# Kernel tuning notes

Hardware: AMD Instinct MI355X
Metric: run time of the kernel (lower is better)

## Reference

```python
import jax, jax.numpy as jnp
import numpy as np

R = 4  # box-filter radius (init kwarg 'radious')


def _diff(c, r, axis):
    # c: cumulative sum along `axis`; returns box-sum along that axis.
    n = c.shape[axis]
    sl = lambda a, b: jax.lax.slice_in_dim(c, a, b, axis=axis)
    left = sl(r, 2 * r + 1)
    middle = sl(2 * r + 1, n) - sl(0, n - 2 * r - 1)
    right = sl(n - 1, n) - sl(n - 2 * r - 1, n - r - 1)
    return jnp.concatenate([left, middle, right], axis=axis)


def _box_filter(x, r):
    # cumsum along H (axis 2) -> windowed diff along H,
    # then cumsum along W (axis 3) -> windowed diff along W.
    return _diff(jnp.cumsum(_diff(jnp.cumsum(x, axis=2), r, axis=2), axis=3), r, axis=3)


def setup_inputs() -> dict:
    key = jax.random.key(0)
    x = jax.random.uniform(key, (8, 3, 1024, 1024), dtype=jnp.float32)
    return {"x": x}


def reference(x) -> jnp.ndarray:
    return _box_filter(x, R)
```

## Files before the change

kernel.cpp:

```cpp
#include <hip/hip_runtime.h>


constexpr int H = 1024, W = 1024;
constexpr int RAD = 4;
constexpr int CHUNK = 16;
constexpr int NCHUNK = H / CHUNK;
constexpr int NIMG = 24;
constexpr int NROWS = CHUNK + 2 * RAD + 1;
constexpr int TPB = 256;

__global__ __launch_bounds__(TPB) void box9_kernel(const float* __restrict__ x,
                                                   float* __restrict__ out) {
    __shared__ float4 Vs[2][TPB + 2];

    const int t     = threadIdx.x;
    const int bid   = blockIdx.x;
    const int chunk = bid & (NCHUNK - 1);
    const int img   = bid >> 6;

    const float* xp = x   + (size_t)img * (H * W) + 4 * t;
    float*       op = out + (size_t)img * (H * W) + 4 * t;
    const int h0 = chunk * CHUNK;

    if (t == 0) {
        Vs[0][0] = make_float4(0.f, 0.f, 0.f, 0.f);
        Vs[1][0] = make_float4(0.f, 0.f, 0.f, 0.f);
    }
    if (t == TPB - 1) {
        Vs[0][TPB + 1] = make_float4(0.f, 0.f, 0.f, 0.f);
        Vs[1][TPB + 1] = make_float4(0.f, 0.f, 0.f, 0.f);
    }

    float4 r[NROWS];
#pragma unroll
    for (int j = 0; j < NROWS; ++j) {
        const int row = h0 - RAD + j;
        r[j] = ((unsigned)row < (unsigned)H)
             ? *reinterpret_cast<const float4*>(xp + (size_t)row * W)
             : make_float4(0.f, 0.f, 0.f, 0.f);
    }

    float4 V = make_float4(0.f, 0.f, 0.f, 0.f);
#pragma unroll
    for (int j = 0; j < 9; ++j) {
        V.x += r[j].x; V.y += r[j].y; V.z += r[j].z; V.w += r[j].w;
    }

#pragma unroll
    for (int j = 0; j < CHUNK; ++j) {
        const int buf = j & 1;
        Vs[buf][t + 1] = V;
        __syncthreads();
        const float4 VL = Vs[buf][t];
        const float4 VR = Vs[buf][t + 2];

        const float T   = V.x + V.y + V.z + V.w;
        const float ls3 = VL.w;
        const float ls2 = ls3 + VL.z;
        const float ls1 = ls2 + VL.y;
        const float lT  = ls1 + VL.x;
        const float rp0 = VR.x;
        const float rp1 = rp0 + VR.y;
        const float rp2 = rp1 + VR.z;
        const float rT  = rp2 + VR.w;

        float4 o;
        o.x = lT  + T + rp0;
        o.y = ls1 + T + rp1;
        o.z = ls2 + T + rp2;
        o.w = ls3 + T + rT;
        *reinterpret_cast<float4*>(op + (size_t)(h0 + j) * W) = o;

        V.x += r[j + 9].x - r[j].x;
        V.y += r[j + 9].y - r[j].y;
        V.z += r[j + 9].z - r[j].z;
        V.w += r[j + 9].w - r[j].w;
    }
}

extern "C" void kernel_launch(void* const* d_in, const int* in_sizes, int n_in,
                              void* d_out, int out_size, void* d_ws, size_t ws_size,
                              hipStream_t stream) {
    const float* x   = (const float*)d_in[0];
    float*       out = (float*)d_out;
    const int n_blocks = NIMG * NCHUNK;
    box9_kernel<<<dim3(n_blocks), dim3(TPB), 0, stream>>>(x, out);
}
```

Baseline: 42.37 us.

## Replace per-row shared-memory halo exchange with wave shuffles and single barrier

Each thread now computes all 16 vertical window sums up front and keeps them in registers. Neighbor sums come from cross-lane shuffles inside each 64-lane wave, and only wave-boundary lanes exchange through small shared arrays. This cuts the 16 per-row __syncthreads barriers to one. The cost is higher register pressure from the 16 extra float4 values, which may lower occupancy, plus 8 shuffles per row.

```diff
diff --git a/kernel.cpp b/kernel.cpp
--- a/kernel.cpp
+++ b/kernel.cpp
@@ -11,25 +11,22 @@
 
 __global__ __launch_bounds__(TPB) void box9_kernel(const float* __restrict__ x,
                                                    float* __restrict__ out) {
-    __shared__ float4 Vs[2][TPB + 2];
+    __shared__ float4 L63s[5][CHUNK];
+    __shared__ float4 L0s[5][CHUNK];
 
-    const int t     = threadIdx.x;
-    const int bid   = blockIdx.x;
+    const int t    = threadIdx.x;
+    const int lane = t & 63;
+    const int wv   = t >> 6;
+    const int bid  = blockIdx.x;
     const int chunk = bid & (NCHUNK - 1);
     const int img   = bid >> 6;
+
+    if (t < CHUNK)               L63s[0][t] = make_float4(0.f, 0.f, 0.f, 0.f);
+    else if (t < 2 * CHUNK)      L0s[4][t - CHUNK] = make_float4(0.f, 0.f, 0.f, 0.f);
 
     const float* xp = x   + (size_t)img * (H * W) + 4 * t;
     float*       op = out + (size_t)img * (H * W) + 4 * t;
     const int h0 = chunk * CHUNK;
-
-    if (t == 0) {
-        Vs[0][0] = make_float4(0.f, 0.f, 0.f, 0.f);
-        Vs[1][0] = make_float4(0.f, 0.f, 0.f, 0.f);
-    }
-    if (t == TPB - 1) {
-        Vs[0][TPB + 1] = make_float4(0.f, 0.f, 0.f, 0.f);
-        Vs[1][TPB + 1] = make_float4(0.f, 0.f, 0.f, 0.f);
-    }
 
     float4 r[NROWS];
 #pragma unroll
@@ -46,15 +43,36 @@
         V.x += r[j].x; V.y += r[j].y; V.z += r[j].z; V.w += r[j].w;
     }
 
+    float4 V16[CHUNK];
 #pragma unroll
     for (int j = 0; j < CHUNK; ++j) {
-        const int buf = j & 1;
-        Vs[buf][t + 1] = V;
-        __syncthreads();
-        const float4 VL = Vs[buf][t];
-        const float4 VR = Vs[buf][t + 2];
+        V16[j] = V;
+        if (lane == 0)  L0s[wv][j]      = V;
+        if (lane == 63) L63s[wv + 1][j] = V;
+        V.x += r[j + 9].x - r[j].x;
+        V.y += r[j + 9].y - r[j].y;
+        V.z += r[j + 9].z - r[j].z;
+        V.w += r[j + 9].w - r[j].w;
+    }
 
-        const float T   = V.x + V.y + V.z + V.w;
+    __syncthreads();
+
+#pragma unroll
+    for (int j = 0; j < CHUNK; ++j) {
+        const float4 Vj = V16[j];
+        float4 VL, VR;
+        VL.x = __shfl(Vj.x, lane - 1);
+        VL.y = __shfl(Vj.y, lane - 1);
+        VL.z = __shfl(Vj.z, lane - 1);
+        VL.w = __shfl(Vj.w, lane - 1);
+        VR.x = __shfl(Vj.x, lane + 1);
+        VR.y = __shfl(Vj.y, lane + 1);
+        VR.z = __shfl(Vj.z, lane + 1);
+        VR.w = __shfl(Vj.w, lane + 1);
+        if (lane == 0)  VL = L63s[wv][j];
+        if (lane == 63) VR = L0s[wv + 1][j];
+
+        const float T   = Vj.x + Vj.y + Vj.z + Vj.w;
         const float ls3 = VL.w;
         const float ls2 = ls3 + VL.z;
         const float ls1 = ls2 + VL.y;
@@ -70,11 +88,6 @@
         o.z = ls2 + T + rp2;
         o.w = ls3 + T + rT;
         *reinterpret_cast<float4*>(op + (size_t)(h0 + j) * W) = o;
-
-        V.x += r[j + 9].x - r[j].x;
-        V.y += r[j + 9].y - r[j].y;
-        V.z += r[j + 9].z - r[j].z;
-        V.w += r[j + 9].w - r[j].w;
     }
 }
 
```

Result: slower. 44.19 us (+4.3%).

## Replace LDS exchange and block barriers with wave shuffles and halo loads

Applied to the files above, without the earlier changes.

Each wavefront now handles an independent 256-column strip, and neighbour column sums are exchanged with __shfl instead of shared memory plus __syncthreads. Edge lanes load an extra halo float4 column and keep a second running sum so strip boundaries stay correct. This removes a block-wide barrier per output row, at the cost of redundant halo loads and extra registers for the r2 array.

```diff
diff --git a/kernel.cpp b/kernel.cpp
--- a/kernel.cpp
+++ b/kernel.cpp
@@ -5,54 +5,66 @@
 constexpr int RAD = 4;
 constexpr int CHUNK = 16;
 constexpr int NCHUNK = H / CHUNK;
+constexpr int NSTRIP = 4;
 constexpr int NIMG = 24;
 constexpr int NROWS = CHUNK + 2 * RAD + 1;
-constexpr int TPB = 256;
+constexpr int HW = H * W;
 
-__global__ __launch_bounds__(TPB) void box9_kernel(const float* __restrict__ x,
+__global__ __launch_bounds__(256) void box9_kernel(const float* __restrict__ x,
                                                    float* __restrict__ out) {
-    __shared__ float4 Vs[2][TPB + 2];
+    const int lane = threadIdx.x & 63;
+    const int wid  = blockIdx.x * 4 + (threadIdx.x >> 6);
 
-    const int t     = threadIdx.x;
-    const int bid   = blockIdx.x;
-    const int chunk = bid & (NCHUNK - 1);
-    const int img   = bid >> 6;
+    const int chunk = wid & (NCHUNK - 1);
+    const int rest  = wid >> 6;
+    const int strip = rest & (NSTRIP - 1);
+    const int img   = rest >> 2;
 
-    const float* xp = x   + (size_t)img * (H * W) + 4 * t;
-    float*       op = out + (size_t)img * (H * W) + 4 * t;
+    const int cs = strip * 256 + 4 * lane;
+    const float* xp = x   + (size_t)img * HW + cs;
+    float*       op = out + (size_t)img * HW + cs;
+
+    const bool isL  = (lane == 0);
+    const bool isR  = (lane == 63);
+    const bool has2 = (isL && strip > 0) || (isR && strip < NSTRIP - 1);
+    const int  cs2  = isL ? (cs - 4) : (cs + 4);
+    const float* xp2 = x + (size_t)img * HW + (has2 ? cs2 : cs);
+
     const int h0 = chunk * CHUNK;
 
-    if (t == 0) {
-        Vs[0][0] = make_float4(0.f, 0.f, 0.f, 0.f);
-        Vs[1][0] = make_float4(0.f, 0.f, 0.f, 0.f);
-    }
-    if (t == TPB - 1) {
-        Vs[0][TPB + 1] = make_float4(0.f, 0.f, 0.f, 0.f);
-        Vs[1][TPB + 1] = make_float4(0.f, 0.f, 0.f, 0.f);
+    float4 r[NROWS], r2[NROWS];
+#pragma unroll
+    for (int j = 0; j < NROWS; ++j) {
+        const int  row = h0 - RAD + j;
+        const bool rok = (unsigned)row < (unsigned)H;
+        r[j] = rok ? *reinterpret_cast<const float4*>(xp + (size_t)row * W)
+                   : make_float4(0.f, 0.f, 0.f, 0.f);
+        r2[j] = (rok && has2)
+              ? *reinterpret_cast<const float4*>(xp2 + (size_t)row * W)
+              : make_float4(0.f, 0.f, 0.f, 0.f);
     }
 
-    float4 r[NROWS];
-#pragma unroll
-    for (int j = 0; j < NROWS; ++j) {
-        const int row = h0 - RAD + j;
-        r[j] = ((unsigned)row < (unsigned)H)
-             ? *reinterpret_cast<const float4*>(xp + (size_t)row * W)
-             : make_float4(0.f, 0.f, 0.f, 0.f);
-    }
-
-    float4 V = make_float4(0.f, 0.f, 0.f, 0.f);
+    float4 V  = make_float4(0.f, 0.f, 0.f, 0.f);
+    float4 V2 = make_float4(0.f, 0.f, 0.f, 0.f);
 #pragma unroll
     for (int j = 0; j < 9; ++j) {
-        V.x += r[j].x; V.y += r[j].y; V.z += r[j].z; V.w += r[j].w;
+        V.x  += r[j].x;  V.y  += r[j].y;  V.z  += r[j].z;  V.w  += r[j].w;
+        V2.x += r2[j].x; V2.y += r2[j].y; V2.z += r2[j].z; V2.w += r2[j].w;
     }
 
 #pragma unroll
     for (int j = 0; j < CHUNK; ++j) {
-        const int buf = j & 1;
-        Vs[buf][t + 1] = V;
-        __syncthreads();
-        const float4 VL = Vs[buf][t];
-        const float4 VR = Vs[buf][t + 2];
+        float4 VL, VR;
+        VL.x = __shfl(V.x, lane - 1);
+        VL.y = __shfl(V.y, lane - 1);
+        VL.z = __shfl(V.z, lane - 1);
+        VL.w = __shfl(V.w, lane - 1);
+        VR.x = __shfl(V.x, lane + 1);
+        VR.y = __shfl(V.y, lane + 1);
+        VR.z = __shfl(V.z, lane + 1);
+        VR.w = __shfl(V.w, lane + 1);
+        if (isL) VL = V2;
+        if (isR) VR = V2;
 
         const float T   = V.x + V.y + V.z + V.w;
         const float ls3 = VL.w;
@@ -71,10 +83,14 @@
         o.w = ls3 + T + rT;
         *reinterpret_cast<float4*>(op + (size_t)(h0 + j) * W) = o;
 
-        V.x += r[j + 9].x - r[j].x;
-        V.y += r[j + 9].y - r[j].y;
-        V.z += r[j + 9].z - r[j].z;
-        V.w += r[j + 9].w - r[j].w;
+        V.x  += r[j + 9].x  - r[j].x;
+        V.y  += r[j + 9].y  - r[j].y;
+        V.z  += r[j + 9].z  - r[j].z;
+        V.w  += r[j + 9].w  - r[j].w;
+        V2.x += r2[j + 9].x - r2[j].x;
+        V2.y += r2[j + 9].y - r2[j].y;
+        V2.z += r2[j + 9].z - r2[j].z;
+        V2.w += r2[j + 9].w - r2[j].w;
     }
 }
 
@@ -83,6 +99,7 @@
                               hipStream_t stream) {
     const float* x   = (const float*)d_in[0];
     float*       out = (float*)d_out;
-    const int n_blocks = NIMG * NCHUNK;
-    box9_kernel<<<dim3(n_blocks), dim3(TPB), 0, stream>>>(x, out);
+    const int n_waves  = NIMG * NSTRIP * NCHUNK;
+    const int n_blocks = n_waves / 4;
+    box9_kernel<<<dim3(n_blocks), dim3(256), 0, stream>>>(x, out);
 }
```

Result: no change. 43.12 us (+1.8%).
